# Optimization experiments

Hardware: AMD Instinct MI355X
Metric: run time of the kernel (lower is better)

## Reference

```python
import jax, jax.numpy as jnp
import numpy as np

K = 7            # neighborhood kernel size
HEADS = 4
DIMS = [64, 64, 64, 64]
POOL = 2
MLP_NAT = 4      # mlp_ratio for NAT layers
MLP_GA = 3       # mlp_ratio for GlobalAttention


def _ln(x, g, b, eps=1e-5):
    m = x.mean(-1, keepdims=True)
    v = ((x - m) ** 2).mean(-1, keepdims=True)
    return (x - m) * jax.lax.rsqrt(v + eps) * g + b


def _nbr(L, k):
    # NATTEN-style clamped window: start in [0, L-k]
    i = jnp.arange(L)
    start = jnp.clip(i - k // 2, 0, L - k)
    idx = start[:, None] + jnp.arange(k)          # [L,k] neighbor coords
    rel = idx - i[:, None] + (k - 1)              # [L,k] rpb index in [0,2k-2]
    return idx, rel


def _nat_attn(x, qkv_w, qkv_b, rpb, proj_w, proj_b):
    B, H, W, C = x.shape
    d = C // HEADS
    qkv = (x @ qkv_w + qkv_b).reshape(B, H, W, 3, HEADS, d)
    q = qkv[..., 0, :, :].transpose(0, 3, 1, 2, 4) * (d ** -0.5)  # [B,h,H,W,d]
    kk = qkv[..., 1, :, :].transpose(0, 3, 1, 2, 4)
    vv = qkv[..., 2, :, :].transpose(0, 3, 1, 2, 4)
    iy, ry = _nbr(H, K)
    ix, rx = _nbr(W, K)
    k_nb = kk[:, :, iy][:, :, :, :, ix]   # [B,h,H,K,W,K,d]
    v_nb = vv[:, :, iy][:, :, :, :, ix]
    attn = jnp.einsum('bhijd,bhiajcd->bhijac', q, k_nb)  # [B,h,H,W,K,K]
    bias = rpb[:, ry][:, :, :, rx]                        # [h,H,K,W,K]
    attn = attn + bias.transpose(0, 1, 3, 2, 4)[None]
    B_, h_, H_, W_ = attn.shape[:4]
    attn = jax.nn.softmax(attn.reshape(B_, h_, H_, W_, K * K), axis=-1)
    attn = attn.reshape(B_, h_, H_, W_, K, K)
    out = jnp.einsum('bhijac,bhiajcd->bhijd', attn, v_nb)
    out = out.transpose(0, 2, 3, 1, 4).reshape(B, H, W, C)
    return out @ proj_w + proj_b


def _nat_block(x, ln1g, ln1b, qw, qb, rpb, pw, pb, ln2g, ln2b, f1w, f1b, f2w, f2b):
    x = x + _nat_attn(_ln(x, ln1g, ln1b), qw, qb, rpb, pw, pb)
    h = _ln(x, ln2g, ln2b)
    h = jax.nn.gelu(h @ f1w + f1b, approximate=False) @ f2w + f2b
    return x + h


def _global_block(x, ln1g, ln1b, qw, qb, ln2g, ln2b, f1w, f1b, f2w, f2b):
    B, H, W, C = x.shape
    d = C // HEADS
    xn = _ln(x, ln1g, ln1b)
    Hp, Wp = H // POOL, W // POOL
    xa = xn.reshape(B, Hp, POOL, Wp, POOL, C).mean((2, 4)).reshape(B, Hp * Wp, C)
    N = Hp * Wp
    qkv = (xa @ qw + qb).reshape(B, N, 3, HEADS, d).transpose(2, 0, 3, 1, 4)
    q, k, v = qkv[0] * (d ** -0.5), qkv[1], qkv[2]
    attn = jax.nn.softmax(jnp.einsum('bhnd,bhmd->bhnm', q, k), axis=-1)
    o = jnp.einsum('bhnm,bhmd->bhnd', attn, v)            # [B,h,N,d]
    o = o.transpose(0, 1, 3, 2).reshape(B, C, Hp, Wp)      # (attn@v).transpose(2,3).reshape(B,C,N)
    o = jnp.repeat(jnp.repeat(o, POOL, axis=2), POOL, axis=3)  # nearest upsample
    x = x + o.transpose(0, 2, 3, 1)
    h = _ln(x, ln2g, ln2b)
    h = jax.nn.gelu(h @ f1w + f1b, approximate=False) @ f2w + f2b
    return x + h


def setup_inputs() -> dict:
    key = jax.random.key(0)
    ks = iter(jax.random.split(key, 32))
    B, H, W = 4, 56, 56
    C = DIMS[0]
    n = len(DIMS) - 1  # 3 NAT branches
    s = 0.02
    inp = {
        'x': jax.random.normal(next(ks), (B, H, W, sum(DIMS)), jnp.float32),
        'nat_ln1_g': jnp.ones((n, C)), 'nat_ln1_b': jnp.zeros((n, C)),
        'nat_qkv_w': jax.random.normal(next(ks), (n, C, 3 * C)) * s,
        'nat_qkv_b': jnp.zeros((n, 3 * C)),
        'nat_rpb': jax.random.normal(next(ks), (n, HEADS, 2 * K - 1, 2 * K - 1)) * s,
        'nat_proj_w': jax.random.normal(next(ks), (n, C, C)) * s,
        'nat_proj_b': jnp.zeros((n, C)),
        'nat_ln2_g': jnp.ones((n, C)), 'nat_ln2_b': jnp.zeros((n, C)),
        'nat_fc1_w': jax.random.normal(next(ks), (n, C, MLP_NAT * C)) * s,
        'nat_fc1_b': jnp.zeros((n, MLP_NAT * C)),
        'nat_fc2_w': jax.random.normal(next(ks), (n, MLP_NAT * C, C)) * s,
        'nat_fc2_b': jnp.zeros((n, C)),
        'ga_ln1_g': jnp.ones((C,)), 'ga_ln1_b': jnp.zeros((C,)),
        'ga_qkv_w': jax.random.normal(next(ks), (C, 3 * C)) * s,
        'ga_qkv_b': jnp.zeros((3 * C,)),
        'ga_ln2_g': jnp.ones((C,)), 'ga_ln2_b': jnp.zeros((C,)),
        'ga_fc1_w': jax.random.normal(next(ks), (C, MLP_GA * C)) * s,
        'ga_fc1_b': jnp.zeros((MLP_GA * C,)),
        'ga_fc2_w': jax.random.normal(next(ks), (MLP_GA * C, C)) * s,
        'ga_fc2_b': jnp.zeros((C,)),
    }
    return inp


def reference(x, nat_ln1_g, nat_ln1_b, nat_qkv_w, nat_qkv_b, nat_rpb, nat_proj_w,
              nat_proj_b, nat_ln2_g, nat_ln2_b, nat_fc1_w, nat_fc1_b, nat_fc2_w,
              nat_fc2_b, ga_ln1_g, ga_ln1_b, ga_qkv_w, ga_qkv_b, ga_ln2_g,
              ga_ln2_b, ga_fc1_w, ga_fc1_b, ga_fc2_w, ga_fc2_b):
    parts = jnp.split(x, np.cumsum(DIMS)[:-1].tolist(), axis=-1)
    outs = []
    for i in range(len(DIMS) - 1):
        outs.append(_nat_block(parts[i], nat_ln1_g[i], nat_ln1_b[i], nat_qkv_w[i],
                               nat_qkv_b[i], nat_rpb[i], nat_proj_w[i], nat_proj_b[i],
                               nat_ln2_g[i], nat_ln2_b[i], nat_fc1_w[i], nat_fc1_b[i],
                               nat_fc2_w[i], nat_fc2_b[i]))
    outs.append(_global_block(parts[-1], ga_ln1_g, ga_ln1_b, ga_qkv_w, ga_qkv_b,
                              ga_ln2_g, ga_ln2_b, ga_fc1_w, ga_fc1_b, ga_fc2_w, ga_fc2_b))
    return jnp.concatenate(outs, axis=-1)
```

## Files before the change

### kernel.cpp

```cpp
#include <hip/hip_runtime.h>
#include <hip/hip_bf16.h>
#include <cstdint>

namespace {

constexpr int NPIX = 12544;

typedef __attribute__((ext_vector_type(8))) short bf16x8;
typedef __attribute__((ext_vector_type(4))) float f32x4;
typedef __attribute__((ext_vector_type(16))) float f32x16;
typedef _Float16 h2 __attribute__((ext_vector_type(2)));

__device__ __forceinline__ float wsum(float v) {
#pragma unroll
  for (int m = 32; m; m >>= 1) v += __shfl_xor(v, m, 64);
  return v;
}

__device__ __forceinline__ uint16_t f2bf(float f) {
  uint32_t u = __builtin_bit_cast(uint32_t, f);
  u += 0x7fffu + ((u >> 16) & 1u);
  return (uint16_t)(u >> 16);
}
__device__ __forceinline__ uint32_t packbf(float a, float b) {
  return (uint32_t)f2bf(a) | ((uint32_t)f2bf(b) << 16);
}
__device__ __forceinline__ ushort f2h(float f) {
  _Float16 h = (_Float16)f;
  return __builtin_bit_cast(ushort, h);
}
__device__ __forceinline__ h2 bch2(uint32_t u) { return __builtin_bit_cast(h2, u); }

__device__ __forceinline__ float gelu_fast(float v) {
  float u = 0.7978845608028654f * (v + 0.044715f * v * v * v);
  float e = __expf(2.f * u);
  float th = 1.f - 2.f * __builtin_amdgcn_rcpf(e + 1.f);
  return 0.5f * v * (1.f + th);
}

__global__ __launch_bounds__(256) void k_prep(
    const float* __restrict__ nqkv, const float* __restrict__ nproj,
    const float* __restrict__ nf1, const float* __restrict__ nf2,
    const float* __restrict__ gqkv, const float* __restrict__ gf1,
    const float* __restrict__ gf2, ushort* __restrict__ wT) {
  int t = blockIdx.x * 256 + threadIdx.x;
  if (t >= 201728) return;
  int i = t;
  if (i < 41472) {
    int br = i / 13824, r = i % 13824, n = r / 72, k = r % 72;
    wT[t] = k < 64 ? f2bf(nqkv[(br * 64 + k) * 192 + n]) : (ushort)0;
    return;
  }
  i -= 41472;
  if (i < 13824) {
    int br = i / 4608, r = i % 4608, n = r / 72, k = r % 72;
    wT[t] = k < 64 ? f2bf(nproj[(br * 64 + k) * 64 + n]) : (ushort)0;
    return;
  }
  i -= 13824;
  if (i < 55296) {
    int br = i / 18432, r = i % 18432, n = r / 72, k = r % 72;
    wT[t] = k < 64 ? f2bf(nf1[(br * 64 + k) * 256 + n]) : (ushort)0;
    return;
  }
  i -= 55296;
  if (i < 50688) {
    int br = i / 16896, r = i % 16896, n = r / 264, k = r % 264;
    wT[t] = k < 256 ? f2bf(nf2[(br * 256 + k) * 64 + n]) : (ushort)0;
    return;
  }
  i -= 50688;
  if (i < 13824) {
    int n = i / 72, k = i % 72;
    wT[t] = k < 64 ? f2bf(gqkv[k * 192 + n]) : (ushort)0;
    return;
  }
  i -= 13824;
  if (i < 13824) {
    int n = i / 72, k = i % 72;
    wT[t] = k < 64 ? f2bf(gf1[k * 192 + n]) : (ushort)0;
    return;
  }
  i -= 13824;
  {
    int n = i / 200, k = i % 200;
    wT[t] = k < 192 ? f2bf(gf2[k * 64 + n]) : (ushort)0;
  }
}

__global__ __launch_bounds__(256) void k_qkv(
    const float* __restrict__ x, const float* __restrict__ nat_ln1_g,
    const float* __restrict__ nat_ln1_b, const ushort* __restrict__ wT,
    const float* __restrict__ nat_qkv_b, ushort* __restrict__ qn,
    ushort* __restrict__ kvn, const float* __restrict__ ga_ln1_g,
    const float* __restrict__ ga_ln1_b, const float* __restrict__ ga_qkv_b,
    ushort* __restrict__ qb, ushort* __restrict__ kb, ushort* __restrict__ vT) {
  __shared__ __align__(16) ushort sA[64 * 72];
  int bid = blockIdx.x;
  int tid = threadIdx.x, lane = tid & 63, wid = tid >> 6;
  if (bid == 637) {
    for (int i = tid; i < 4096; i += 256) {
      int bh = i >> 8, rem = i & 255;
      int n = 784 + (rem >> 4), d = rem & 15;
      qb[((size_t)bh * 800 + n) * 16 + d] = 0;
      kb[((size_t)bh * 800 + n) * 16 + d] = 0;
      vT[((size_t)bh * 16 + d) * 800 + n] = 0;
    }
    return;
  }
  int lr = lane & 15, lk = (lane >> 4) * 8;
  if (bid < 588) {
    int br = bid / 196, grp = bid % 196;
    const ushort* Wg = wT + br * 13824;
    float g = nat_ln1_g[br * 64 + lane], bb = nat_ln1_b[br * 64 + lane];
#pragma unroll
    for (int i = 0; i < 16; ++i) {
      int pl = wid * 16 + i;
      float v = x[(size_t)(grp * 64 + pl) * 256 + br * 64 + lane];
      float s1 = wsum(v), s2 = wsum(v * v);
      float m = s1 * (1.f / 64.f);
      float var = s2 * (1.f / 64.f) - m * m;
      sA[pl * 72 + lane] = f2bf((v - m) * rsqrtf(var + 1e-5f) * g + bb);
    }
    __syncthreads();
    int m0 = wid * 16;
    bf16x8 a0 = *(const bf16x8*)&sA[(m0 + lr) * 72 + lk];
    bf16x8 a1 = *(const bf16x8*)&sA[(m0 + lr) * 72 + 32 + lk];
    int r0 = m0 + (lane >> 4) * 4;
#pragma unroll
    for (int nt = 0; nt < 12; ++nt) {
      int n0 = nt * 16;
      bf16x8 b0 = *(const bf16x8*)&Wg[(n0 + lr) * 72 + lk];
      bf16x8 b1 = *(const bf16x8*)&Wg[(n0 + lr) * 72 + 32 + lk];
      f32x4 acc = {0.f, 0.f, 0.f, 0.f};
      acc = __builtin_amdgcn_mfma_f32_16x16x32_bf16(a0, b0, acc, 0, 0, 0);
      acc = __builtin_amdgcn_mfma_f32_16x16x32_bf16(a1, b1, acc, 0, 0, 0);
      int col = n0 + lr;
      float bias = nat_qkv_b[br * 192 + col];
      if (nt < 4) {
        ushort* op = qn + ((size_t)br * NPIX + grp * 64 + r0) * 64 + col;
#pragma unroll
        for (int r = 0; r < 4; ++r) op[r * 64] = f2h((acc[r] + bias) * 0.25f);
      } else {
        ushort* op = kvn + ((size_t)br * NPIX + grp * 64 + r0) * 128 + (col - 64);
#pragma unroll
        for (int r = 0; r < 4; ++r) op[r * 128] = f2h(acc[r] + bias);
      }
    }
  } else {
    int g64 = bid - 588;
    const ushort* Wg = wT + 161280;
    float gg = ga_ln1_g[lane], bb = ga_ln1_b[lane];
#pragma unroll
    for (int i = 0; i < 16; ++i) {
      int tl = wid * 16 + i;
      int token = g64 * 64 + tl;
      int b = token / 784, rem2 = token % 784, hp = rem2 / 28, wp = rem2 % 28;
      float s = 0.f;
#pragma unroll
      for (int dy = 0; dy < 2; ++dy)
#pragma unroll
        for (int dxx = 0; dxx < 2; ++dxx) {
          int pix = b * 3136 + (hp * 2 + dy) * 56 + (wp * 2 + dxx);
          float v = x[(size_t)pix * 256 + 192 + lane];
          float s1 = wsum(v), s2 = wsum(v * v);
          float m = s1 * (1.f / 64.f);
          float var = s2 * (1.f / 64.f) - m * m;
          s += (v - m) * rsqrtf(var + 1e-5f) * gg + bb;
        }
      sA[tl * 72 + lane] = f2bf(0.25f * s);
    }
    __syncthreads();
    int m0 = wid * 16;
    bf16x8 a0 = *(const bf16x8*)&sA[(m0 + lr) * 72 + lk];
    bf16x8 a1 = *(const bf16x8*)&sA[(m0 + lr) * 72 + 32 + lk];
    int r0 = m0 + (lane >> 4) * 4;
#pragma unroll
    for (int nt = 0; nt < 12; ++nt) {
      int n0 = nt * 16;
      bf16x8 b0 = *(const bf16x8*)&Wg[(n0 + lr) * 72 + lk];
      bf16x8 b1 = *(const bf16x8*)&Wg[(n0 + lr) * 72 + 32 + lk];
      f32x4 acc = {0.f, 0.f, 0.f, 0.f};
      acc = __builtin_amdgcn_mfma_f32_16x16x32_bf16(a0, b0, acc, 0, 0, 0);
      acc = __builtin_amdgcn_mfma_f32_16x16x32_bf16(a1, b1, acc, 0, 0, 0);
      int col = n0 + lr;
      float bias = ga_qkv_b[col];
      int hh = (col & 63) >> 4, d = col & 15;
#pragma unroll
      for (int r = 0; r < 4; ++r) {
        int token = g64 * 64 + r0 + r;
        int b = token / 784, nn = token % 784;
        float v = acc[r] + bias;
        if (col < 64)
          qb[((size_t)(b * 4 + hh) * 800 + nn) * 16 + d] = f2bf(v * 0.25f);
        else if (col < 128)
          kb[((size_t)(b * 4 + hh) * 800 + nn) * 16 + d] = f2bf(v);
        else
          vT[((size_t)(b * 4 + hh) * 16 + d) * 800 + nn] = f2bf(v);
      }
    }
  }
}

__global__ __launch_bounds__(256) void k_attn(
    const ushort* __restrict__ qn, const ushort* __restrict__ kvn,
    const float* __restrict__ rpb, const ushort* __restrict__ wT,
    const float* __restrict__ pb, const float* __restrict__ x,
    float* __restrict__ x1, const ushort* __restrict__ qb,
    const ushort* __restrict__ kb, const ushort* __restrict__ vT,
    float* __restrict__ x1g) {
  __shared__ __align__(16) ushort sBuf[196 * 136];
  int bid = blockIdx.x;
  int tid = threadIdx.x, lane = tid & 63, wid = tid >> 6;
  if (bid < 588) {
    ushort* sKV = sBuf;
    int br = bid / 196, rem = bid % 196;
    int b = rem / 49, t = rem % 49;
    int y0 = (t / 7) * 8, x0 = (t % 7) * 8;
    int hy = min(max(y0 - 3, 0), 42), hx = min(max(x0 - 3, 0), 42);
    const ushort* kvbase = kvn + ((size_t)br * NPIX + b * 3136) * 128;
    for (int i = tid; i < 3136; i += 256) {
      int p = i >> 4, c = i & 15;
      int py = p / 14, px = p % 14;
      int gp = (hy + py) * 56 + (hx + px);
      uint4 v = *(const uint4*)&kvbase[(size_t)gp * 128 + c * 8];
      *(uint4*)&sKV[p * 136 + c * 8] = v;
    }
    __syncthreads();
    int pl = tid & 63, h = tid >> 6;
    int ly = pl >> 3, lx = pl & 7;
    int y = y0 + ly, xg = x0 + lx;
    int sy = min(max(y - 3, 0), 49), sx = min(max(xg - 3, 0), 49);
    int by = sy - hy, bx = sx - hx;
    int gpix = b * 3136 + y * 56 + xg;
    const ushort* qp = qn + ((size_t)br * NPIX + gpix) * 64 + h * 16;
    uint4 qv0 = *(const uint4*)&qp[0];
    uint4 qv1 = *(const uint4*)&qp[8];
    h2 q[8] = {bch2(qv0.x), bch2(qv0.y), bch2(qv0.z), bch2(qv0.w),
               bch2(qv1.x), bch2(qv1.y), bch2(qv1.z), bch2(qv1.w)};
    const float* rp = rpb + (br * 4 + h) * 169 + (sy - y + 6) * 13 + (sx - xg + 6);
    h2 z = {(_Float16)0.f, (_Float16)0.f};
    float s[49];
    float mx = -1e30f;
#pragma unroll
    for (int a = 0; a < 7; ++a) {
      const ushort* krow = &sKV[((by + a) * 14 + bx) * 136 + h * 16];
      const float* rpa = rp + a * 13;
#pragma unroll
      for (int c = 0; c < 7; ++c) {
        const ushort* kp = krow + c * 136;
        uint4 k0 = *(const uint4*)&kp[0];
        uint4 k1 = *(const uint4*)&kp[8];
        h2 d = z;
        d = bch2(k0.x) * q[0] + d;
        d = bch2(k0.y) * q[1] + d;
        d = bch2(k0.z) * q[2] + d;
        d = bch2(k0.w) * q[3] + d;
        d = bch2(k1.x) * q[4] + d;
        d = bch2(k1.y) * q[5] + d;
        d = bch2(k1.z) * q[6] + d;
        d = bch2(k1.w) * q[7] + d;
        float sd = (float)d[0] + (float)d[1] + rpa[c];
        s[a * 7 + c] = sd;
        mx = fmaxf(mx, sd);
      }
    }
    float l = 0.f;
    h2 acc[8];
#pragma unroll
    for (int i = 0; i < 8; ++i) acc[i] = z;
#pragma unroll
    for (int a = 0; a < 7; ++a) {
      const ushort* vrow = &sKV[((by + a) * 14 + bx) * 136 + h * 16 + 64];
#pragma unroll
      for (int c = 0; c < 7; ++c) {
        float p = __expf(s[a * 7 + c] - mx);
        l += p;
        h2 p2 = {(_Float16)p, (_Float16)p};
        const ushort* vp = vrow + c * 136;
        uint4 v0 = *(const uint4*)&vp[0];
        uint4 v1 = *(const uint4*)&vp[8];
        acc[0] = bch2(v0.x) * p2 + acc[0];
        acc[1] = bch2(v0.y) * p2 + acc[1];
        acc[2] = bch2(v0.z) * p2 + acc[2];
        acc[3] = bch2(v0.w) * p2 + acc[3];
        acc[4] = bch2(v1.x) * p2 + acc[4];
        acc[5] = bch2(v1.y) * p2 + acc[5];
        acc[6] = bch2(v1.z) * p2 + acc[6];
        acc[7] = bch2(v1.w) * p2 + acc[7];
      }
    }
    float inv = 1.f / l;
    __syncthreads();
    ushort* sAp = sBuf;
    uint32_t* ao = (uint32_t*)&sAp[pl * 72 + h * 16];
#pragma unroll
    for (int i = 0; i < 8; ++i)
      ao[i] = packbf((float)acc[i][0] * inv, (float)acc[i][1] * inv);
    __syncthreads();
    const ushort* Wp = wT + 41472 + br * 4608;
    int lr = lane & 15, lk = (lane >> 4) * 8;
    int m0 = wid * 16;
    bf16x8 a0 = *(const bf16x8*)&sAp[(m0 + lr) * 72 + lk];
    bf16x8 a1 = *(const bf16x8*)&sAp[(m0 + lr) * 72 + 32 + lk];
    int r0 = m0 + (lane >> 4) * 4;
#pragma unroll
    for (int nt = 0; nt < 4; ++nt) {
      int n0 = nt * 16;
      bf16x8 b0 = *(const bf16x8*)&Wp[(n0 + lr) * 72 + lk];
      bf16x8 b1 = *(const bf16x8*)&Wp[(n0 + lr) * 72 + 32 + lk];
      f32x4 oacc = {0.f, 0.f, 0.f, 0.f};
      oacc = __builtin_amdgcn_mfma_f32_16x16x32_bf16(a0, b0, oacc, 0, 0, 0);
      oacc = __builtin_amdgcn_mfma_f32_16x16x32_bf16(a1, b1, oacc, 0, 0, 0);
      int col = n0 + lr;
      float bias = pb[br * 64 + col];
#pragma unroll
      for (int r = 0; r < 4; ++r) {
        int rr = r0 + r;
        int gp2 = b * 3136 + (y0 + (rr >> 3)) * 56 + (x0 + (rr & 7));
        x1[((size_t)br * NPIX + gp2) * 64 + col] =
            oacc[r] + bias + x[(size_t)gp2 * 256 + br * 64 + col];
      }
    }
  } else {
    int wt = (bid - 588) * 4 + wid;
    int bh = wt / 25, qt = wt % 25;
    int h = bh & 3, b = bh >> 2;
    int qrow = lane & 31, hi = lane >> 5;
    int dmod = lane & 15;
    const ushort* qbase = qb + (size_t)bh * 800 * 16;
    const ushort* kbase = kb + (size_t)bh * 800 * 16;
    const ushort* vbase = vT + (size_t)bh * 16 * 800 + (size_t)dmod * 800;
    bf16x8 qf = *(const bf16x8*)&qbase[(qt * 32 + qrow) * 16 + hi * 8];
    float m = -1e30f, l = 0.f;
    f32x16 acc_o;
#pragma unroll
    for (int r = 0; r < 16; ++r) acc_o[r] = 0.f;
    bf16x8 kf = *(const bf16x8*)&kbase[(0 + qrow) * 16 + hi * 8];
    bf16x8 vf0 = *(const bf16x8*)&vbase[0 + hi * 8];
    bf16x8 vf1 = *(const bf16x8*)&vbase[16 + hi * 8];
    for (int kt = 0; kt < 25; ++kt) {
      int nb = (kt < 24 ? kt + 1 : 24) * 32;
      bf16x8 nkf = *(const bf16x8*)&kbase[(nb + qrow) * 16 + hi * 8];
      bf16x8 nvf0 = *(const bf16x8*)&vbase[nb + hi * 8];
      bf16x8 nvf1 = *(const bf16x8*)&vbase[nb + 16 + hi * 8];
      f32x16 zero;
#pragma unroll
      for (int r = 0; r < 16; ++r) zero[r] = 0.f;
      f32x16 st = __builtin_amdgcn_mfma_f32_32x32x16_bf16(kf, qf, zero, 0, 0, 0);
      float s[16];
#pragma unroll
      for (int r = 0; r < 16; ++r) s[r] = st[r];
      if (kt == 24) {
#pragma unroll
        for (int r = 8; r < 16; ++r) s[r] = -1e30f;
      }
      float tm = s[0];
#pragma unroll
      for (int r = 1; r < 16; ++r) tm = fmaxf(tm, s[r]);
      tm = fmaxf(tm, __shfl_xor(tm, 32, 64));
      if (__any(tm > m + 8.f)) {
        float mn = fmaxf(m, tm);
        float sc = __expf(m - mn);
        l *= sc;
        m = mn;
#pragma unroll
        for (int r = 0; r < 16; ++r) {
          int row = (r & 3) + 4 * hi + 8 * (r >> 2);
          float scr = __shfl(sc, row, 64);
          acc_o[r] *= scr;
        }
      }
      uint32_t pk[8];
      float ps = 0.f;
#pragma unroll
      for (int i = 0; i < 8; ++i) {
        float p0 = __expf(s[2 * i] - m), p1 = __expf(s[2 * i + 1] - m);
        ps += p0 + p1;
        pk[i] = packbf(p0, p1);
      }
      l += ps;
#pragma unroll
      for (int t = 0; t < 2; ++t) {
        uint32_t c0 = pk[4 * t + 0], c1 = pk[4 * t + 1];
        uint32_t c2 = pk[4 * t + 2], c3 = pk[4 * t + 3];
        uint32_t b00 = __shfl((int)c0, qrow, 64), b02 = __shfl((int)c2, qrow, 64);
        uint32_t b10 = __shfl((int)c1, qrow, 64), b12 = __shfl((int)c3, qrow, 64);
        uint32_t b20 = __shfl((int)c0, qrow + 32, 64), b22 = __shfl((int)c2, qrow + 32, 64);
        uint32_t b30 = __shfl((int)c1, qrow + 32, 64), b32 = __shfl((int)c3, qrow + 32, 64);
        union { uint32_t u[4]; bf16x8 v; } pa;
        pa.u[0] = hi ? b02 : b00;
        pa.u[1] = hi ? b12 : b10;
        pa.u[2] = hi ? b22 : b20;
        pa.u[3] = hi ? b32 : b30;
        acc_o = __builtin_amdgcn_mfma_f32_32x32x16_bf16(pa.v, (t ? vf1 : vf0),
                                                        acc_o, 0, 0, 0);
      }
      kf = nkf; vf0 = nvf0; vf1 = nvf1;
    }
    l += __shfl_xor(l, 32, 64);
    float inv = 1.f / l;
#pragma unroll
    for (int r = 0; r < 16; ++r) {
      int row = (r & 3) + 4 * hi + 8 * (r >> 2);
      float invr = __shfl(inv, row, 64);
      int n = qt * 32 + row;
      if (n < 784 && qrow < 16) {
        float o = acc_o[r] * invr;
        int hp = n / 28, wp = n % 28;
        int ch = h * 16 + dmod;
#pragma unroll
        for (int dy = 0; dy < 2; ++dy)
#pragma unroll
          for (int dxx = 0; dxx < 2; ++dxx) {
            int pix = b * 3136 + (hp * 2 + dy) * 56 + (wp * 2 + dxx);
            x1g[(size_t)pix * 64 + ch] = x[(size_t)pix * 256 + 192 + ch] + o;
          }
      }
    }
  }
}

template <bool NAT>
__device__ __forceinline__ void mlp_body(
    int br, int grp, ushort* sX, ushort* sH,
    const float* __restrict__ x1, const ushort* __restrict__ W1,
    const ushort* __restrict__ W2, const float* __restrict__ B1,
    const float* __restrict__ B2, const float* __restrict__ G,
    const float* __restrict__ Bt, float* __restrict__ out) {
  constexpr int H1 = NAT ? 256 : 192;
  constexpr int K2P = NAT ? 264 : 200;
  constexpr int KB = H1 / 32;
  int tid = threadIdx.x, lane = tid & 63, wid = tid >> 6;
  const float* xin = x1 + ((size_t)br * NPIX + grp * 64) * 64;
  float g = G[lane], bb = Bt[lane];
#pragma unroll
  for (int i = 0; i < 16; ++i) {
    int pl = wid * 16 + i;
    float v = xin[pl * 64 + lane];
    float s1 = wsum(v), s2 = wsum(v * v);
    float m = s1 * (1.f / 64.f);
    float var = s2 * (1.f / 64.f) - m * m;
    sX[pl * 72 + lane] = f2bf((v - m) * rsqrtf(var + 1e-5f) * g + bb);
  }
  __syncthreads();
  int lr = lane & 15, lk = (lane >> 4) * 8;
  int mbase = (wid & 1) * 16;
  int r0 = (lane >> 4) * 4;
  bf16x8 a0[2], a1[2];
#pragma unroll
  for (int mh = 0; mh < 2; ++mh) {
    int m0 = mh * 32 + mbase;
    a0[mh] = *(const bf16x8*)&sX[(m0 + lr) * 72 + lk];
    a1[mh] = *(const bf16x8*)&sX[(m0 + lr) * 72 + 32 + lk];
  }
#pragma unroll
  for (int t2 = 0; t2 < H1 / 32; ++t2) {
    int n0 = ((wid >> 1) + 2 * t2) * 16;
    bf16x8 b0 = *(const bf16x8*)&W1[(n0 + lr) * 72 + lk];
    bf16x8 b1 = *(const bf16x8*)&W1[(n0 + lr) * 72 + 32 + lk];
    int col = n0 + lr;
    float b1v = B1[col];
#pragma unroll
    for (int mh = 0; mh < 2; ++mh) {
      f32x4 acc = {0.f, 0.f, 0.f, 0.f};
      acc = __builtin_amdgcn_mfma_f32_16x16x32_bf16(a0[mh], b0, acc, 0, 0, 0);
      acc = __builtin_amdgcn_mfma_f32_16x16x32_bf16(a1[mh], b1, acc, 0, 0, 0);
      int m0 = mh * 32 + mbase;
#pragma unroll
      for (int r = 0; r < 4; ++r) {
        int row = m0 + r0 + r;
        sH[row * K2P + (col ^ (((row >> 2) & 3) << 3))] =
            f2bf(gelu_fast(acc[r] + b1v));
      }
    }
  }
  __syncthreads();
#pragma unroll
  for (int mh = 0; mh < 2; ++mh) {
    int m0 = mh * 32 + mbase;
    bf16x8 af[KB];
#pragma unroll
    for (int kb = 0; kb < KB; ++kb) {
      int arow = m0 + lr;
      af[kb] = *(const bf16x8*)&sH[arow * K2P +
                                   ((kb * 32 + lk) ^ (((arow >> 2) & 3) << 3))];
    }
#pragma unroll
    for (int u = 0; u < 2; ++u) {
      int n0 = ((wid >> 1) + 2 * u) * 16;
      f32x4 acc = {0.f, 0.f, 0.f, 0.f};
#pragma unroll
      for (int kb = 0; kb < KB; ++kb) {
        bf16x8 bf = *(const bf16x8*)&W2[(n0 + lr) * K2P + kb * 32 + lk];
        acc = __builtin_amdgcn_mfma_f32_16x16x32_bf16(af[kb], bf, acc, 0, 0, 0);
      }
      int col = n0 + lr;
      float b2v = B2[col];
#pragma unroll
      for (int r = 0; r < 4; ++r) {
        int p = m0 + r0 + r;
        int pix = grp * 64 + p;
        out[(size_t)pix * 256 + br * 64 + col] = xin[p * 64 + col] + acc[r] + b2v;
      }
    }
  }
}

__global__ __launch_bounds__(256) void k_mlp(
    const float* __restrict__ x1, const float* __restrict__ nat_ln2_g,
    const float* __restrict__ nat_ln2_b, const ushort* __restrict__ wT,
    const float* __restrict__ nat_f1b, const float* __restrict__ nat_f2b,
    const float* __restrict__ ga_ln2_g, const float* __restrict__ ga_ln2_b,
    const float* __restrict__ ga_f1b, const float* __restrict__ ga_f2b,
    float* __restrict__ out) {
  __shared__ __align__(16) ushort sX[64 * 72];
  __shared__ __align__(16) ushort sH[64 * 264];
  int bid = blockIdx.x;
  if (bid < 588) {
    int br = bid / 196, grp = bid % 196;
    mlp_body<true>(br, grp, sX, sH, x1, wT + 55296 + br * 18432,
                   wT + 110592 + br * 16896, nat_f1b + br * 256,
                   nat_f2b + br * 64, nat_ln2_g + br * 64, nat_ln2_b + br * 64,
                   out);
  } else {
    int grp = bid - 588;
    mlp_body<false>(3, grp, sX, sH, x1, wT + 175104, wT + 188928, ga_f1b,
                    ga_f2b, ga_ln2_g, ga_ln2_b, out);
  }
}

}

extern "C" void kernel_launch(void* const* d_in, const int* in_sizes, int n_in,
                              void* d_out, int out_size, void* d_ws, size_t ws_size,
                              hipStream_t stream) {
  const float* x = (const float*)d_in[0];
  const float* nat_ln1_g = (const float*)d_in[1];
  const float* nat_ln1_b = (const float*)d_in[2];
  const float* nat_qkv_w = (const float*)d_in[3];
  const float* nat_qkv_b = (const float*)d_in[4];
  const float* nat_rpb = (const float*)d_in[5];
  const float* nat_proj_w = (const float*)d_in[6];
  const float* nat_proj_b = (const float*)d_in[7];
  const float* nat_ln2_g = (const float*)d_in[8];
  const float* nat_ln2_b = (const float*)d_in[9];
  const float* nat_fc1_w = (const float*)d_in[10];
  const float* nat_fc1_b = (const float*)d_in[11];
  const float* nat_fc2_w = (const float*)d_in[12];
  const float* nat_fc2_b = (const float*)d_in[13];
  const float* ga_ln1_g = (const float*)d_in[14];
  const float* ga_ln1_b = (const float*)d_in[15];
  const float* ga_qkv_w = (const float*)d_in[16];
  const float* ga_qkv_b = (const float*)d_in[17];
  const float* ga_ln2_g = (const float*)d_in[18];
  const float* ga_ln2_b = (const float*)d_in[19];
  const float* ga_fc1_w = (const float*)d_in[20];
  const float* ga_fc1_b = (const float*)d_in[21];
  const float* ga_fc2_w = (const float*)d_in[22];
  const float* ga_fc2_b = (const float*)d_in[23];

  uint8_t* w8 = (uint8_t*)d_ws;
  ushort* qn  = (ushort*)w8;
  ushort* kvn = (ushort*)(w8 + 4816896);
  float*  x1  = (float*)(w8 + 14450688);
  ushort* wT  = (ushort*)(w8 + 27295744);
  ushort* qgb = (ushort*)(w8 + 27699200);
  ushort* kgb = (ushort*)(w8 + 28108800);
  ushort* vgT = (ushort*)(w8 + 28518400);

  k_prep<<<dim3(789), dim3(256), 0, stream>>>(nat_qkv_w, nat_proj_w, nat_fc1_w,
                                              nat_fc2_w, ga_qkv_w, ga_fc1_w,
                                              ga_fc2_w, wT);
  k_qkv<<<dim3(638), dim3(256), 0, stream>>>(x, nat_ln1_g, nat_ln1_b, wT,
                                             nat_qkv_b, qn, kvn, ga_ln1_g,
                                             ga_ln1_b, ga_qkv_b, qgb, kgb, vgT);
  k_attn<<<dim3(688), dim3(256), 0, stream>>>(qn, kvn, nat_rpb, wT, nat_proj_b,
                                              x, x1, qgb, kgb, vgT,
                                              x1 + (size_t)3 * NPIX * 64);
  k_mlp<<<dim3(784), dim3(256), 0, stream>>>(x1, nat_ln2_g, nat_ln2_b, wT,
                                             nat_fc1_b, nat_fc2_b, ga_ln2_g,
                                             ga_ln2_b, ga_fc1_b, ga_fc2_b,
                                             (float*)d_out);
}
```

Before: 85.15 us.

## Fuse NAT LN2+MLP into attention kernel, keep residual in shared memory

The NAT branch now runs LayerNorm2, fc1+GELU and fc2 inside the attention kernel right after the projection, keeping the residual x1 tile in shared memory as fp16 and writing the final output directly. This removes the fp32 x1 round trip through global memory and one kernel launch for the NAT branches. The global-attention branch's MLP moves to a separate smaller kernel. The trade-off is more work and shared memory pressure per attention block, which may lower occupancy. The residual is also stored in fp16 rather than fp32, which costs some precision.

```diff
diff --git a/kernel.cpp b/kernel.cpp
--- a/kernel.cpp
+++ b/kernel.cpp
@@ -28,6 +28,9 @@
 __device__ __forceinline__ ushort f2h(float f) {
   _Float16 h = (_Float16)f;
   return __builtin_bit_cast(ushort, h);
+}
+__device__ __forceinline__ float h2f(ushort u) {
+  return (float)__builtin_bit_cast(_Float16, u);
 }
 __device__ __forceinline__ h2 bch2(uint32_t u) { return __builtin_bit_cast(h2, u); }
 
@@ -206,7 +209,9 @@
     const ushort* __restrict__ qn, const ushort* __restrict__ kvn,
     const float* __restrict__ rpb, const ushort* __restrict__ wT,
     const float* __restrict__ pb, const float* __restrict__ x,
-    float* __restrict__ x1, const ushort* __restrict__ qb,
+    const float* __restrict__ nat_ln2_g, const float* __restrict__ nat_ln2_b,
+    const float* __restrict__ nat_f1b, const float* __restrict__ nat_f2b,
+    float* __restrict__ out, const ushort* __restrict__ qb,
     const ushort* __restrict__ kb, const ushort* __restrict__ vT,
     float* __restrict__ x1g) {
   __shared__ __align__(16) ushort sBuf[196 * 136];
@@ -292,34 +297,115 @@
     }
     float inv = 1.f / l;
     __syncthreads();
-    ushort* sAp = sBuf;
-    uint32_t* ao = (uint32_t*)&sAp[pl * 72 + h * 16];
+    ushort* sX  = sBuf;
+    ushort* sH  = sBuf + 4608;
+    ushort* x1f = sBuf + 21504;
+    uint32_t* ao = (uint32_t*)&x1f[pl * 72 + h * 16];
 #pragma unroll
     for (int i = 0; i < 8; ++i)
       ao[i] = packbf((float)acc[i][0] * inv, (float)acc[i][1] * inv);
     __syncthreads();
     const ushort* Wp = wT + 41472 + br * 4608;
     int lr = lane & 15, lk = (lane >> 4) * 8;
-    int m0 = wid * 16;
-    bf16x8 a0 = *(const bf16x8*)&sAp[(m0 + lr) * 72 + lk];
-    bf16x8 a1 = *(const bf16x8*)&sAp[(m0 + lr) * 72 + 32 + lk];
-    int r0 = m0 + (lane >> 4) * 4;
-#pragma unroll
-    for (int nt = 0; nt < 4; ++nt) {
-      int n0 = nt * 16;
-      bf16x8 b0 = *(const bf16x8*)&Wp[(n0 + lr) * 72 + lk];
-      bf16x8 b1 = *(const bf16x8*)&Wp[(n0 + lr) * 72 + 32 + lk];
-      f32x4 oacc = {0.f, 0.f, 0.f, 0.f};
-      oacc = __builtin_amdgcn_mfma_f32_16x16x32_bf16(a0, b0, oacc, 0, 0, 0);
-      oacc = __builtin_amdgcn_mfma_f32_16x16x32_bf16(a1, b1, oacc, 0, 0, 0);
+    {
+      int m0 = wid * 16;
+      bf16x8 a0 = *(const bf16x8*)&x1f[(m0 + lr) * 72 + lk];
+      bf16x8 a1 = *(const bf16x8*)&x1f[(m0 + lr) * 72 + 32 + lk];
+      int r0 = m0 + (lane >> 4) * 4;
+#pragma unroll
+      for (int nt = 0; nt < 4; ++nt) {
+        int n0 = nt * 16;
+        bf16x8 b0 = *(const bf16x8*)&Wp[(n0 + lr) * 72 + lk];
+        bf16x8 b1 = *(const bf16x8*)&Wp[(n0 + lr) * 72 + 32 + lk];
+        f32x4 oacc = {0.f, 0.f, 0.f, 0.f};
+        oacc = __builtin_amdgcn_mfma_f32_16x16x32_bf16(a0, b0, oacc, 0, 0, 0);
+        oacc = __builtin_amdgcn_mfma_f32_16x16x32_bf16(a1, b1, oacc, 0, 0, 0);
+        int col = n0 + lr;
+        float bias = pb[br * 64 + col];
+#pragma unroll
+        for (int r = 0; r < 4; ++r) {
+          int rr = r0 + r;
+          int gp2 = b * 3136 + (y0 + (rr >> 3)) * 56 + (x0 + (rr & 7));
+          x1f[rr * 72 + col] =
+              f2h(oacc[r] + bias + x[(size_t)gp2 * 256 + br * 64 + col]);
+        }
+      }
+    }
+    __syncthreads();
+    float g2 = nat_ln2_g[br * 64 + lane], b2l = nat_ln2_b[br * 64 + lane];
+#pragma unroll
+    for (int i = 0; i < 16; ++i) {
+      int p = wid * 16 + i;
+      float v = h2f(x1f[p * 72 + lane]);
+      float s1 = wsum(v), s2 = wsum(v * v);
+      float m = s1 * (1.f / 64.f);
+      float var = s2 * (1.f / 64.f) - m * m;
+      sX[p * 72 + lane] = f2bf((v - m) * rsqrtf(var + 1e-5f) * g2 + b2l);
+    }
+    __syncthreads();
+    const ushort* W1 = wT + 55296 + br * 18432;
+    const ushort* W2 = wT + 110592 + br * 16896;
+    const float* B1 = nat_f1b + br * 256;
+    const float* B2 = nat_f2b + br * 64;
+    int mbase = (wid & 1) * 16;
+    int r0 = (lane >> 4) * 4;
+    bf16x8 a0m[2], a1m[2];
+#pragma unroll
+    for (int mh = 0; mh < 2; ++mh) {
+      int m0 = mh * 32 + mbase;
+      a0m[mh] = *(const bf16x8*)&sX[(m0 + lr) * 72 + lk];
+      a1m[mh] = *(const bf16x8*)&sX[(m0 + lr) * 72 + 32 + lk];
+    }
+#pragma unroll
+    for (int t2 = 0; t2 < 8; ++t2) {
+      int n0 = ((wid >> 1) + 2 * t2) * 16;
+      bf16x8 b0 = *(const bf16x8*)&W1[(n0 + lr) * 72 + lk];
+      bf16x8 b1 = *(const bf16x8*)&W1[(n0 + lr) * 72 + 32 + lk];
       int col = n0 + lr;
-      float bias = pb[br * 64 + col];
-#pragma unroll
-      for (int r = 0; r < 4; ++r) {
-        int rr = r0 + r;
-        int gp2 = b * 3136 + (y0 + (rr >> 3)) * 56 + (x0 + (rr & 7));
-        x1[((size_t)br * NPIX + gp2) * 64 + col] =
-            oacc[r] + bias + x[(size_t)gp2 * 256 + br * 64 + col];
+      float b1v = B1[col];
+#pragma unroll
+      for (int mh = 0; mh < 2; ++mh) {
+        f32x4 facc = {0.f, 0.f, 0.f, 0.f};
+        facc = __builtin_amdgcn_mfma_f32_16x16x32_bf16(a0m[mh], b0, facc, 0, 0, 0);
+        facc = __builtin_amdgcn_mfma_f32_16x16x32_bf16(a1m[mh], b1, facc, 0, 0, 0);
+        int m0 = mh * 32 + mbase;
+#pragma unroll
+        for (int r = 0; r < 4; ++r) {
+          int row = m0 + r0 + r;
+          sH[row * 264 + (col ^ (((row >> 2) & 3) << 3))] =
+              f2bf(gelu_fast(facc[r] + b1v));
+        }
+      }
+    }
+    __syncthreads();
+#pragma unroll
+    for (int mh = 0; mh < 2; ++mh) {
+      int m0 = mh * 32 + mbase;
+      bf16x8 af[8];
+#pragma unroll
+      for (int kb2 = 0; kb2 < 8; ++kb2) {
+        int arow = m0 + lr;
+        af[kb2] = *(const bf16x8*)&sH[arow * 264 +
+                                      ((kb2 * 32 + lk) ^ (((arow >> 2) & 3) << 3))];
+      }
+#pragma unroll
+      for (int u = 0; u < 2; ++u) {
+        int n0 = ((wid >> 1) + 2 * u) * 16;
+        f32x4 facc = {0.f, 0.f, 0.f, 0.f};
+#pragma unroll
+        for (int kb2 = 0; kb2 < 8; ++kb2) {
+          bf16x8 bf = *(const bf16x8*)&W2[(n0 + lr) * 264 + kb2 * 32 + lk];
+          facc = __builtin_amdgcn_mfma_f32_16x16x32_bf16(af[kb2], bf, facc, 0, 0, 0);
+        }
+        int col = n0 + lr;
+        float b2v = B2[col];
+#pragma unroll
+        for (int r = 0; r < 4; ++r) {
+          int p = m0 + r0 + r;
+          int gp2 = b * 3136 + (y0 + (p >> 3)) * 56 + (x0 + (p & 7));
+          out[(size_t)gp2 * 256 + br * 64 + col] =
+              h2f(x1f[p * 72 + col]) + facc[r] + b2v;
+        }
       }
     }
   } else {
@@ -421,19 +507,22 @@
   }
 }
 
-template <bool NAT>
-__device__ __forceinline__ void mlp_body(
-    int br, int grp, ushort* sX, ushort* sH,
-    const float* __restrict__ x1, const ushort* __restrict__ W1,
-    const ushort* __restrict__ W2, const float* __restrict__ B1,
-    const float* __restrict__ B2, const float* __restrict__ G,
-    const float* __restrict__ Bt, float* __restrict__ out) {
-  constexpr int H1 = NAT ? 256 : 192;
-  constexpr int K2P = NAT ? 264 : 200;
-  constexpr int KB = H1 / 32;
+__global__ __launch_bounds__(256) void k_mlp_ga(
+    const float* __restrict__ x1g, const ushort* __restrict__ wT,
+    const float* __restrict__ ga_ln2_g, const float* __restrict__ ga_ln2_b,
+    const float* __restrict__ ga_f1b, const float* __restrict__ ga_f2b,
+    float* __restrict__ out) {
+  constexpr int H1 = 192;
+  constexpr int K2P = 200;
+  constexpr int KB = 6;
+  __shared__ __align__(16) ushort sX[64 * 72];
+  __shared__ __align__(16) ushort sH[64 * 200];
+  int grp = blockIdx.x;
   int tid = threadIdx.x, lane = tid & 63, wid = tid >> 6;
-  const float* xin = x1 + ((size_t)br * NPIX + grp * 64) * 64;
-  float g = G[lane], bb = Bt[lane];
+  const ushort* W1 = wT + 175104;
+  const ushort* W2 = wT + 188928;
+  const float* xin = x1g + (size_t)(grp * 64) * 64;
+  float g = ga_ln2_g[lane], bb = ga_ln2_b[lane];
 #pragma unroll
   for (int i = 0; i < 16; ++i) {
     int pl = wid * 16 + i;
@@ -460,7 +549,7 @@
     bf16x8 b0 = *(const bf16x8*)&W1[(n0 + lr) * 72 + lk];
     bf16x8 b1 = *(const bf16x8*)&W1[(n0 + lr) * 72 + 32 + lk];
     int col = n0 + lr;
-    float b1v = B1[col];
+    float b1v = ga_f1b[col];
 #pragma unroll
     for (int mh = 0; mh < 2; ++mh) {
       f32x4 acc = {0.f, 0.f, 0.f, 0.f};
@@ -496,37 +585,14 @@
         acc = __builtin_amdgcn_mfma_f32_16x16x32_bf16(af[kb], bf, acc, 0, 0, 0);
       }
       int col = n0 + lr;
-      float b2v = B2[col];
+      float b2v = ga_f2b[col];
 #pragma unroll
       for (int r = 0; r < 4; ++r) {
         int p = m0 + r0 + r;
         int pix = grp * 64 + p;
-        out[(size_t)pix * 256 + br * 64 + col] = xin[p * 64 + col] + acc[r] + b2v;
-      }
-    }
-  }
-}
-
-__global__ __launch_bounds__(256) void k_mlp(
-    const float* __restrict__ x1, const float* __restrict__ nat_ln2_g,
-    const float* __restrict__ nat_ln2_b, const ushort* __restrict__ wT,
-    const float* __restrict__ nat_f1b, const float* __restrict__ nat_f2b,
-    const float* __restrict__ ga_ln2_g, const float* __restrict__ ga_ln2_b,
-    const float* __restrict__ ga_f1b, const float* __restrict__ ga_f2b,
-    float* __restrict__ out) {
-  __shared__ __align__(16) ushort sX[64 * 72];
-  __shared__ __align__(16) ushort sH[64 * 264];
-  int bid = blockIdx.x;
-  if (bid < 588) {
-    int br = bid / 196, grp = bid % 196;
-    mlp_body<true>(br, grp, sX, sH, x1, wT + 55296 + br * 18432,
-                   wT + 110592 + br * 16896, nat_f1b + br * 256,
-                   nat_f2b + br * 64, nat_ln2_g + br * 64, nat_ln2_b + br * 64,
-                   out);
-  } else {
-    int grp = bid - 588;
-    mlp_body<false>(3, grp, sX, sH, x1, wT + 175104, wT + 188928, ga_f1b,
-                    ga_f2b, ga_ln2_g, ga_ln2_b, out);
+        out[(size_t)pix * 256 + 192 + col] = xin[p * 64 + col] + acc[r] + b2v;
+      }
+    }
   }
 }
 
@@ -563,11 +629,11 @@
   uint8_t* w8 = (uint8_t*)d_ws;
   ushort* qn  = (ushort*)w8;
   ushort* kvn = (ushort*)(w8 + 4816896);
-  float*  x1  = (float*)(w8 + 14450688);
-  ushort* wT  = (ushort*)(w8 + 27295744);
-  ushort* qgb = (ushort*)(w8 + 27699200);
-  ushort* kgb = (ushort*)(w8 + 28108800);
-  ushort* vgT = (ushort*)(w8 + 28518400);
+  float*  x1g = (float*)(w8 + 14450688);
+  ushort* wT  = (ushort*)(w8 + 17661952);
+  ushort* qgb = (ushort*)(w8 + 18065408);
+  ushort* kgb = (ushort*)(w8 + 18475008);
+  ushort* vgT = (ushort*)(w8 + 18884608);
 
   k_prep<<<dim3(789), dim3(256), 0, stream>>>(nat_qkv_w, nat_proj_w, nat_fc1_w,
                                               nat_fc2_w, ga_qkv_w, ga_fc1_w,
@@ -575,11 +641,10 @@
   k_qkv<<<dim3(638), dim3(256), 0, stream>>>(x, nat_ln1_g, nat_ln1_b, wT,
                                              nat_qkv_b, qn, kvn, ga_ln1_g,
                                              ga_ln1_b, ga_qkv_b, qgb, kgb, vgT);
-  k_attn<<<dim3(688), dim3(256), 0, stream>>>(qn, kvn, nat_rpb, wT, nat_proj_b,
-                                              x, x1, qgb, kgb, vgT,
-                                              x1 + (size_t)3 * NPIX * 64);
-  k_mlp<<<dim3(784), dim3(256), 0, stream>>>(x1, nat_ln2_g, nat_ln2_b, wT,
-                                             nat_fc1_b, nat_fc2_b, ga_ln2_g,
-                                             ga_ln2_b, ga_fc1_b, ga_fc2_b,
-                                             (float*)d_out);
-}
+  k_attn<<<dim3(688), dim3(256), 0, stream>>>(
+      qn, kvn, nat_rpb, wT, nat_proj_b, x, nat_ln2_g, nat_ln2_b, nat_fc1_b,
+      nat_fc2_b, (float*)d_out, qgb, kgb, vgT, x1g);
+  k_mlp_ga<<<dim3(196), dim3(256), 0, stream>>>(x1g, wT, ga_ln2_g, ga_ln2_b,
+                                                ga_fc1_b, ga_fc2_b,
+                                                (float*)d_out);
+}
```

Result: slower. 92.14 us (+8.2%).

## Give each attention head a wave-private LDS tile and drop block barriers

Applied to the files above, without the earlier changes.

The neighborhood-attention path now gives each wave (one head) its own LDS region holding only that head's 16 channels. It loads K first, then overwrites the same region with V after the scores are computed. This removes the block-wide __syncthreads and shrinks LDS use, which should let more blocks stay resident. The cost is two separate, narrower global gather passes per wave (32-byte pieces instead of full 256-byte rows). Correctness also relies on intra-wave LDS ordering with no explicit barrier or fence.

```diff
diff --git a/kernel.cpp b/kernel.cpp
--- a/kernel.cpp
+++ b/kernel.cpp
@@ -209,46 +209,44 @@
     float* __restrict__ x1, const ushort* __restrict__ qb,
     const ushort* __restrict__ kb, const ushort* __restrict__ vT,
     float* __restrict__ x1g) {
-  __shared__ __align__(16) ushort sBuf[196 * 136];
+  __shared__ __align__(16) ushort sKV[4 * 196 * 16];
+  __shared__ __align__(16) ushort sAp[64 * 72];
   int bid = blockIdx.x;
   int tid = threadIdx.x, lane = tid & 63, wid = tid >> 6;
   if (bid < 588) {
-    ushort* sKV = sBuf;
     int br = bid / 196, rem = bid % 196;
     int b = rem / 49, t = rem % 49;
     int y0 = (t / 7) * 8, x0 = (t % 7) * 8;
     int hy = min(max(y0 - 3, 0), 42), hx = min(max(x0 - 3, 0), 42);
-    const ushort* kvbase = kvn + ((size_t)br * NPIX + b * 3136) * 128;
-    for (int i = tid; i < 3136; i += 256) {
-      int p = i >> 4, c = i & 15;
-      int py = p / 14, px = p % 14;
+    const ushort* kvh = kvn + ((size_t)br * NPIX + b * 3136) * 128 + wid * 16;
+    ushort* sKh = sKV + wid * 3136;
+    for (int i = lane; i < 392; i += 64) {
+      int row = i >> 1, half = (i & 1) * 8;
+      int py = row / 14, px = row % 14;
       int gp = (hy + py) * 56 + (hx + px);
-      uint4 v = *(const uint4*)&kvbase[(size_t)gp * 128 + c * 8];
-      *(uint4*)&sKV[p * 136 + c * 8] = v;
-    }
-    __syncthreads();
-    int pl = tid & 63, h = tid >> 6;
-    int ly = pl >> 3, lx = pl & 7;
+      *(uint4*)&sKh[row * 16 + half] = *(const uint4*)&kvh[(size_t)gp * 128 + half];
+    }
+    int ly = lane >> 3, lx = lane & 7;
     int y = y0 + ly, xg = x0 + lx;
     int sy = min(max(y - 3, 0), 49), sx = min(max(xg - 3, 0), 49);
     int by = sy - hy, bx = sx - hx;
     int gpix = b * 3136 + y * 56 + xg;
-    const ushort* qp = qn + ((size_t)br * NPIX + gpix) * 64 + h * 16;
+    const ushort* qp = qn + ((size_t)br * NPIX + gpix) * 64 + wid * 16;
     uint4 qv0 = *(const uint4*)&qp[0];
     uint4 qv1 = *(const uint4*)&qp[8];
     h2 q[8] = {bch2(qv0.x), bch2(qv0.y), bch2(qv0.z), bch2(qv0.w),
                bch2(qv1.x), bch2(qv1.y), bch2(qv1.z), bch2(qv1.w)};
-    const float* rp = rpb + (br * 4 + h) * 169 + (sy - y + 6) * 13 + (sx - xg + 6);
+    const float* rp = rpb + (br * 4 + wid) * 169 + (sy - y + 6) * 13 + (sx - xg + 6);
     h2 z = {(_Float16)0.f, (_Float16)0.f};
     float s[49];
     float mx = -1e30f;
 #pragma unroll
     for (int a = 0; a < 7; ++a) {
-      const ushort* krow = &sKV[((by + a) * 14 + bx) * 136 + h * 16];
+      const ushort* krow = &sKh[((by + a) * 14 + bx) * 16];
       const float* rpa = rp + a * 13;
 #pragma unroll
       for (int c = 0; c < 7; ++c) {
-        const ushort* kp = krow + c * 136;
+        const ushort* kp = krow + c * 16;
         uint4 k0 = *(const uint4*)&kp[0];
         uint4 k1 = *(const uint4*)&kp[8];
         h2 d = z;
@@ -265,19 +263,26 @@
         mx = fmaxf(mx, sd);
       }
     }
+    for (int i = lane; i < 392; i += 64) {
+      int row = i >> 1, half = (i & 1) * 8;
+      int py = row / 14, px = row % 14;
+      int gp = (hy + py) * 56 + (hx + px);
+      *(uint4*)&sKh[row * 16 + half] =
+          *(const uint4*)&kvh[(size_t)gp * 128 + 64 + half];
+    }
     float l = 0.f;
     h2 acc[8];
 #pragma unroll
     for (int i = 0; i < 8; ++i) acc[i] = z;
 #pragma unroll
     for (int a = 0; a < 7; ++a) {
-      const ushort* vrow = &sKV[((by + a) * 14 + bx) * 136 + h * 16 + 64];
+      const ushort* vrow = &sKh[((by + a) * 14 + bx) * 16];
 #pragma unroll
       for (int c = 0; c < 7; ++c) {
         float p = __expf(s[a * 7 + c] - mx);
         l += p;
         h2 p2 = {(_Float16)p, (_Float16)p};
-        const ushort* vp = vrow + c * 136;
+        const ushort* vp = vrow + c * 16;
         uint4 v0 = *(const uint4*)&vp[0];
         uint4 v1 = *(const uint4*)&vp[8];
         acc[0] = bch2(v0.x) * p2 + acc[0];
@@ -291,9 +296,7 @@
       }
     }
     float inv = 1.f / l;
-    __syncthreads();
-    ushort* sAp = sBuf;
-    uint32_t* ao = (uint32_t*)&sAp[pl * 72 + h * 16];
+    uint32_t* ao = (uint32_t*)&sAp[lane * 72 + wid * 16];
 #pragma unroll
     for (int i = 0; i < 8; ++i)
       ao[i] = packbf((float)acc[i][0] * inv, (float)acc[i][1] * inv);
```

Measured after the change: 104.6 us. 22.8% more time.

## Process two horizontal pixels per thread sharing K/V loads with online softmax

Applied to the files above, without the earlier changes.

Each thread in the neighborhood-attention stage now handles two adjacent pixels of one head, walking a union window of width 7 or 8 so each K/V row read from shared memory serves both queries. Scores are folded into an online softmax with running max and rescaling, so the 49-entry score array is no longer kept. Only half the threads (128 of 256) do attention, and the loops are no longer fully unrolled, adding data-dependent branches and rescale work per step, which can hurt occupancy use and ILP.

```diff
diff --git a/kernel.cpp b/kernel.cpp
--- a/kernel.cpp
+++ b/kernel.cpp
@@ -223,87 +223,126 @@
       int p = i >> 4, c = i & 15;
       int py = p / 14, px = p % 14;
       int gp = (hy + py) * 56 + (hx + px);
-      uint4 v = *(const uint4*)&kvbase[(size_t)gp * 128 + c * 8];
-      *(uint4*)&sKV[p * 136 + c * 8] = v;
+      *(uint4*)&sKV[p * 136 + c * 8] =
+          *(const uint4*)&kvbase[(size_t)gp * 128 + c * 8];
     }
     __syncthreads();
-    int pl = tid & 63, h = tid >> 6;
-    int ly = pl >> 3, lx = pl & 7;
-    int y = y0 + ly, xg = x0 + lx;
-    int sy = min(max(y - 3, 0), 49), sx = min(max(xg - 3, 0), 49);
-    int by = sy - hy, bx = sx - hx;
-    int gpix = b * 3136 + y * 56 + xg;
-    const ushort* qp = qn + ((size_t)br * NPIX + gpix) * 64 + h * 16;
-    uint4 qv0 = *(const uint4*)&qp[0];
-    uint4 qv1 = *(const uint4*)&qp[8];
-    h2 q[8] = {bch2(qv0.x), bch2(qv0.y), bch2(qv0.z), bch2(qv0.w),
-               bch2(qv1.x), bch2(qv1.y), bch2(qv1.z), bch2(qv1.w)};
-    const float* rp = rpb + (br * 4 + h) * 169 + (sy - y + 6) * 13 + (sx - xg + 6);
     h2 z = {(_Float16)0.f, (_Float16)0.f};
-    float s[49];
-    float mx = -1e30f;
-#pragma unroll
-    for (int a = 0; a < 7; ++a) {
-      const ushort* krow = &sKV[((by + a) * 14 + bx) * 136 + h * 16];
-      const float* rpa = rp + a * 13;
-#pragma unroll
-      for (int c = 0; c < 7; ++c) {
-        const ushort* kp = krow + c * 136;
-        uint4 k0 = *(const uint4*)&kp[0];
-        uint4 k1 = *(const uint4*)&kp[8];
-        h2 d = z;
-        d = bch2(k0.x) * q[0] + d;
-        d = bch2(k0.y) * q[1] + d;
-        d = bch2(k0.z) * q[2] + d;
-        d = bch2(k0.w) * q[3] + d;
-        d = bch2(k1.x) * q[4] + d;
-        d = bch2(k1.y) * q[5] + d;
-        d = bch2(k1.z) * q[6] + d;
-        d = bch2(k1.w) * q[7] + d;
-        float sd = (float)d[0] + (float)d[1] + rpa[c];
-        s[a * 7 + c] = sd;
-        mx = fmaxf(mx, sd);
-      }
-    }
-    float l = 0.f;
-    h2 acc[8];
-#pragma unroll
-    for (int i = 0; i < 8; ++i) acc[i] = z;
-#pragma unroll
-    for (int a = 0; a < 7; ++a) {
-      const ushort* vrow = &sKV[((by + a) * 14 + bx) * 136 + h * 16 + 64];
-#pragma unroll
-      for (int c = 0; c < 7; ++c) {
-        float p = __expf(s[a * 7 + c] - mx);
-        l += p;
-        h2 p2 = {(_Float16)p, (_Float16)p};
-        const ushort* vp = vrow + c * 136;
-        uint4 v0 = *(const uint4*)&vp[0];
-        uint4 v1 = *(const uint4*)&vp[8];
-        acc[0] = bch2(v0.x) * p2 + acc[0];
-        acc[1] = bch2(v0.y) * p2 + acc[1];
-        acc[2] = bch2(v0.z) * p2 + acc[2];
-        acc[3] = bch2(v0.w) * p2 + acc[3];
-        acc[4] = bch2(v1.x) * p2 + acc[4];
-        acc[5] = bch2(v1.y) * p2 + acc[5];
-        acc[6] = bch2(v1.z) * p2 + acc[6];
-        acc[7] = bch2(v1.w) * p2 + acc[7];
-      }
-    }
-    float inv = 1.f / l;
+    h2 acc0[8], acc1[8];
+#pragma unroll
+    for (int i = 0; i < 8; ++i) { acc0[i] = z; acc1[i] = z; }
+    float l0 = 0.f, l1 = 0.f;
+    int h = tid >> 5, pr = tid & 31;
+    int ly = pr >> 2, pxc = (pr & 3) * 2;
+    int pl0 = ly * 8 + pxc;
+    if (tid < 128) {
+      int y = y0 + ly;
+      int xg0 = x0 + pxc, xg1 = xg0 + 1;
+      int sy = min(max(y - 3, 0), 49);
+      int sx0 = min(max(xg0 - 3, 0), 49), sx1 = min(max(xg1 - 3, 0), 49);
+      int dx1 = sx1 - sx0;
+      int by = sy - hy, bx = sx0 - hx;
+      int gp0 = b * 3136 + y * 56 + xg0;
+      const ushort* qp = qn + ((size_t)br * NPIX + gp0) * 64 + h * 16;
+      uint4 q0a = *(const uint4*)&qp[0];
+      uint4 q0b = *(const uint4*)&qp[8];
+      uint4 q1a = *(const uint4*)&qp[64];
+      uint4 q1b = *(const uint4*)&qp[72];
+      h2 q0[8] = {bch2(q0a.x), bch2(q0a.y), bch2(q0a.z), bch2(q0a.w),
+                  bch2(q0b.x), bch2(q0b.y), bch2(q0b.z), bch2(q0b.w)};
+      h2 q1[8] = {bch2(q1a.x), bch2(q1a.y), bch2(q1a.z), bch2(q1a.w),
+                  bch2(q1b.x), bch2(q1b.y), bch2(q1b.z), bch2(q1b.w)};
+      const float* rp0 =
+          rpb + (br * 4 + h) * 169 + (sy - y + 6) * 13 + (sx0 - xg0 + 6);
+      const float* rp1 =
+          rpb + (br * 4 + h) * 169 + (sy - y + 6) * 13 + (sx1 - xg1 + 6);
+      float m0 = -1e30f, m1 = -1e30f;
+      int cmax = 7 + dx1;
+      for (int a = 0; a < 7; ++a) {
+        const ushort* krow = &sKV[((by + a) * 14 + bx) * 136 + h * 16];
+        const float* rp0a = rp0 + a * 13;
+        const float* rp1a = rp1 + a * 13;
+        for (int c = 0; c < cmax; ++c) {
+          const ushort* kp = krow + c * 136;
+          uint4 k0 = *(const uint4*)&kp[0];
+          uint4 k1 = *(const uint4*)&kp[8];
+          uint4 v0 = *(const uint4*)&kp[64];
+          uint4 v1 = *(const uint4*)&kp[72];
+          h2 d0 = z, d1 = z;
+          h2 kk;
+          kk = bch2(k0.x); d0 = kk * q0[0] + d0; d1 = kk * q1[0] + d1;
+          kk = bch2(k0.y); d0 = kk * q0[1] + d0; d1 = kk * q1[1] + d1;
+          kk = bch2(k0.z); d0 = kk * q0[2] + d0; d1 = kk * q1[2] + d1;
+          kk = bch2(k0.w); d0 = kk * q0[3] + d0; d1 = kk * q1[3] + d1;
+          kk = bch2(k1.x); d0 = kk * q0[4] + d0; d1 = kk * q1[4] + d1;
+          kk = bch2(k1.y); d0 = kk * q0[5] + d0; d1 = kk * q1[5] + d1;
+          kk = bch2(k1.z); d0 = kk * q0[6] + d0; d1 = kk * q1[6] + d1;
+          kk = bch2(k1.w); d0 = kk * q0[7] + d0; d1 = kk * q1[7] + d1;
+          if (c < 7) {
+            float sd = (float)d0[0] + (float)d0[1] + rp0a[c];
+            if (sd > m0) {
+              float sc = __expf(m0 - sd);
+              m0 = sd; l0 *= sc;
+              h2 sc2 = {(_Float16)sc, (_Float16)sc};
+#pragma unroll
+              for (int i = 0; i < 8; ++i) acc0[i] = acc0[i] * sc2;
+            }
+            float p = __expf(sd - m0);
+            l0 += p;
+            h2 p2 = {(_Float16)p, (_Float16)p};
+            acc0[0] = bch2(v0.x) * p2 + acc0[0];
+            acc0[1] = bch2(v0.y) * p2 + acc0[1];
+            acc0[2] = bch2(v0.z) * p2 + acc0[2];
+            acc0[3] = bch2(v0.w) * p2 + acc0[3];
+            acc0[4] = bch2(v1.x) * p2 + acc0[4];
+            acc0[5] = bch2(v1.y) * p2 + acc0[5];
+            acc0[6] = bch2(v1.z) * p2 + acc0[6];
+            acc0[7] = bch2(v1.w) * p2 + acc0[7];
+          }
+          int c1 = c - dx1;
+          if (c1 >= 0 && c1 < 7) {
+            float sd = (float)d1[0] + (float)d1[1] + rp1a[c1];
+            if (sd > m1) {
+              float sc = __expf(m1 - sd);
+              m1 = sd; l1 *= sc;
+              h2 sc2 = {(_Float16)sc, (_Float16)sc};
+#pragma unroll
+              for (int i = 0; i < 8; ++i) acc1[i] = acc1[i] * sc2;
+            }
+            float p = __expf(sd - m1);
+            l1 += p;
+            h2 p2 = {(_Float16)p, (_Float16)p};
+            acc1[0] = bch2(v0.x) * p2 + acc1[0];
+            acc1[1] = bch2(v0.y) * p2 + acc1[1];
+            acc1[2] = bch2(v0.z) * p2 + acc1[2];
+            acc1[3] = bch2(v0.w) * p2 + acc1[3];
+            acc1[4] = bch2(v1.x) * p2 + acc1[4];
+            acc1[5] = bch2(v1.y) * p2 + acc1[5];
+            acc1[6] = bch2(v1.z) * p2 + acc1[6];
+            acc1[7] = bch2(v1.w) * p2 + acc1[7];
+          }
+        }
+      }
+    }
     __syncthreads();
     ushort* sAp = sBuf;
-    uint32_t* ao = (uint32_t*)&sAp[pl * 72 + h * 16];
-#pragma unroll
-    for (int i = 0; i < 8; ++i)
-      ao[i] = packbf((float)acc[i][0] * inv, (float)acc[i][1] * inv);
+    if (tid < 128) {
+      float i0 = 1.f / l0, i1 = 1.f / l1;
+      uint32_t* ao0 = (uint32_t*)&sAp[pl0 * 72 + h * 16];
+      uint32_t* ao1 = (uint32_t*)&sAp[(pl0 + 1) * 72 + h * 16];
+#pragma unroll
+      for (int i = 0; i < 8; ++i) {
+        ao0[i] = packbf((float)acc0[i][0] * i0, (float)acc0[i][1] * i0);
+        ao1[i] = packbf((float)acc1[i][0] * i1, (float)acc1[i][1] * i1);
+      }
+    }
     __syncthreads();
     const ushort* Wp = wT + 41472 + br * 4608;
     int lr = lane & 15, lk = (lane >> 4) * 8;
-    int m0 = wid * 16;
-    bf16x8 a0 = *(const bf16x8*)&sAp[(m0 + lr) * 72 + lk];
-    bf16x8 a1 = *(const bf16x8*)&sAp[(m0 + lr) * 72 + 32 + lk];
-    int r0 = m0 + (lane >> 4) * 4;
+    int m0r = wid * 16;
+    bf16x8 a0 = *(const bf16x8*)&sAp[(m0r + lr) * 72 + lk];
+    bf16x8 a1 = *(const bf16x8*)&sAp[(m0r + lr) * 72 + 32 + lk];
+    int r0 = m0r + (lane >> 4) * 4;
 #pragma unroll
     for (int nt = 0; nt < 4; ++nt) {
       int n0 = nt * 16;
```

Measured after the change: 93.56 us. 9.9% more time.
